# Performance work log

Measured on AMD Instinct MI355X. Metric: run time of the kernel, lower is better.

## Reference

```python
import jax, jax.numpy as jnp
import numpy as np

# Placement region / binning constants (match init_kwargs)
XL, YL, XH, YH = 0.0, 0.0, 512.0, 512.0
NBX, NBY = 512, 512
BSX = (XH - XL) / NBX  # 1.0
BSY = (YH - YL) / NBY  # 1.0
N = 5_000_000  # num_movable_nodes


def setup_inputs() -> dict:
    key = jax.random.key(0)
    k1, k2, k3, k4 = jax.random.split(key, 4)
    # pos = [x_0..x_{N-1}, y_0..y_{N-1}]; keep nodes inside the region
    pos = jax.random.uniform(k1, (2 * N,), jnp.float32) * (XH - 1.0)
    # LUT/FF instances are smaller than one bin -> at most a 2x2 bin window
    node_size_x = jax.random.uniform(k2, (N,), jnp.float32) * 0.9 + 0.05
    node_size_y = jax.random.uniform(k3, (N,), jnp.float32) * 0.9 + 0.05
    utilization_map = jax.random.uniform(k4, (NBX, NBY), jnp.float32) * 2.0
    flop_lut_indices = jnp.arange(N, dtype=jnp.int32)
    return {"pos": pos, "node_size_x": node_size_x, "node_size_y": node_size_y,
            "utilization_map": utilization_map, "flop_lut_indices": flop_lut_indices}


def _route_area(pos, sx, sy, umap):
    x = pos[:N]
    y = pos[N:2 * N]
    x_hi = x + sx
    y_hi = y + sy
    # lowest overlapped bin index per node
    bx0 = jnp.clip(jnp.floor((x - XL) / BSX).astype(jnp.int32), 0, NBX - 1)
    by0 = jnp.clip(jnp.floor((y - YL) / BSY).astype(jnp.int32), 0, NBY - 1)
    area = jnp.zeros((N,), jnp.float32)
    # node extent < bin size => at most a 2x2 window of bins overlaps each node
    for dx in range(2):
        bx = bx0 + dx
        bxl = XL + bx.astype(jnp.float32) * BSX
        ox = jnp.clip(jnp.minimum(x_hi, bxl + BSX) - jnp.maximum(x, bxl), 0.0, None)
        ox = jnp.where(bx < NBX, ox, 0.0)
        bxc = jnp.minimum(bx, NBX - 1)
        for dy in range(2):
            by = by0 + dy
            byl = YL + by.astype(jnp.float32) * BSY
            oy = jnp.clip(jnp.minimum(y_hi, byl + BSY) - jnp.maximum(y, byl), 0.0, None)
            oy = jnp.where(by < NBY, oy, 0.0)
            byc = jnp.minimum(by, NBY - 1)
            # irregular gather from the 2D utilization map
            area = area + ox * oy * umap[bxc, byc]
    return area


def reference(pos, node_size_x, node_size_y, utilization_map, flop_lut_indices):
    area = _route_area(pos, node_size_x, node_size_y, utilization_map)
    # only flop/lut instances receive a route area; others stay zero
    out = jnp.zeros((N,), jnp.float32).at[flop_lut_indices].set(area[flop_lut_indices])
    return out
```

## Files before the change

kernel.cpp:

```cpp
#include <hip/hip_runtime.h>

#define NBX 512
#define NBY 512

__global__ __launch_bounds__(256) void build_table_kernel(
    const float* __restrict__ u, float4* __restrict__ W)
{
    int t = blockIdx.x * blockDim.x + threadIdx.x;
    int bx = t >> 9;
    int by = t & 511;
    int bxp = bx + 1 < NBX ? bx + 1 : NBX - 1;
    int byp = by + 1 < NBY ? by + 1 : NBY - 1;
    float a = u[(bx  << 9) | by ];
    float b = u[(bx  << 9) | byp];
    float c = u[(bxp << 9) | by ];
    float d = u[(bxp << 9) | byp];
    W[t] = make_float4(a, b, c, d);
}

__device__ __forceinline__ float node_area(float x, float y, float sx, float sy,
                                           const float4* __restrict__ W)
{
    float x_hi = x + sx;
    float y_hi = y + sy;

    int bx0 = (int)floorf(x);
    bx0 = bx0 < 0 ? 0 : (bx0 > NBX - 1 ? NBX - 1 : bx0);
    int by0 = (int)floorf(y);
    by0 = by0 < 0 ? 0 : (by0 > NBY - 1 ? NBY - 1 : by0);

    float bx0f = (float)bx0;
    float by0f = (float)by0;

    float ox0 = fmaxf(fminf(x_hi, bx0f + 1.0f) - fmaxf(x, bx0f), 0.0f);
    float ox1 = fmaxf(fminf(x_hi, bx0f + 2.0f) - fmaxf(x, bx0f + 1.0f), 0.0f);
    if (bx0 + 1 >= NBX) ox1 = 0.0f;

    float oy0 = fmaxf(fminf(y_hi, by0f + 1.0f) - fmaxf(y, by0f), 0.0f);
    float oy1 = fmaxf(fminf(y_hi, by0f + 2.0f) - fmaxf(y, by0f + 1.0f), 0.0f);
    if (by0 + 1 >= NBY) oy1 = 0.0f;

    float4 w = W[(bx0 << 9) | by0];

    float area = ox0 * oy0 * w.x;
    area = fmaf(ox0 * oy1, w.y, area);
    area = fmaf(ox1 * oy0, w.z, area);
    area = fmaf(ox1 * oy1, w.w, area);
    return area;
}

__global__ __launch_bounds__(256) void route_area_v2_kernel(
    const float*  __restrict__ pos,
    const float*  __restrict__ nsx,
    const float*  __restrict__ nsy,
    const float4* __restrict__ W,
    const int*    __restrict__ idx,
    float*        __restrict__ out,
    int n)
{
    int t = blockIdx.x * blockDim.x + threadIdx.x;
    int base = t * 4;
    if (base >= n) return;

    if (base + 3 < n) {
        int4 j4 = *(const int4*)(idx + base);
        if (j4.x == base && j4.y == base + 1 && j4.z == base + 2 && j4.w == base + 3) {
            float4 x4  = *(const float4*)(pos + base);
            float4 y4  = *(const float4*)(pos + n + base);
            float4 sx4 = *(const float4*)(nsx + base);
            float4 sy4 = *(const float4*)(nsy + base);

            float4 r;
            r.x = node_area(x4.x, y4.x, sx4.x, sy4.x, W);
            r.y = node_area(x4.y, y4.y, sx4.y, sy4.y, W);
            r.z = node_area(x4.z, y4.z, sx4.z, sy4.z, W);
            r.w = node_area(x4.w, y4.w, sx4.w, sy4.w, W);

            *(float4*)(out + base) = r;
            return;
        }
    }

    #pragma unroll
    for (int k = 0; k < 4; ++k) {
        int i = base + k;
        if (i >= n) break;
        int j = idx[i];
        float x  = pos[j];
        float y  = pos[n + j];
        float sx = nsx[j];
        float sy = nsy[j];
        out[j] = node_area(x, y, sx, sy, W);
    }
}

__global__ __launch_bounds__(256) void route_area_v1_kernel(
    const float* __restrict__ pos,
    const float* __restrict__ nsx,
    const float* __restrict__ nsy,
    const float* __restrict__ umap,
    const int*   __restrict__ idx,
    float*       __restrict__ out,
    int n)
{
    int i = blockIdx.x * blockDim.x + threadIdx.x;
    if (i >= n) return;

    int j = idx[i];
    float x  = pos[j];
    float y  = pos[n + j];
    float sx = nsx[j];
    float sy = nsy[j];
    float x_hi = x + sx;
    float y_hi = y + sy;

    int bx0 = (int)floorf(x);
    bx0 = bx0 < 0 ? 0 : (bx0 > NBX - 1 ? NBX - 1 : bx0);
    int by0 = (int)floorf(y);
    by0 = by0 < 0 ? 0 : (by0 > NBY - 1 ? NBY - 1 : by0);

    float area = 0.0f;
    #pragma unroll
    for (int dx = 0; dx < 2; ++dx) {
        int bx = bx0 + dx;
        float bxl = (float)bx;
        float ox = fmaxf(fminf(x_hi, bxl + 1.0f) - fmaxf(x, bxl), 0.0f);
        if (bx >= NBX) ox = 0.0f;
        int bxc = bx < NBX - 1 ? bx : NBX - 1;
        #pragma unroll
        for (int dy = 0; dy < 2; ++dy) {
            int by = by0 + dy;
            float byl = (float)by;
            float oy = fmaxf(fminf(y_hi, byl + 1.0f) - fmaxf(y, byl), 0.0f);
            if (by >= NBY) oy = 0.0f;
            int byc = by < NBY - 1 ? by : NBY - 1;
            area = fmaf(ox * oy, umap[bxc * NBY + byc], area);
        }
    }
    out[j] = area;
}

extern "C" void kernel_launch(void* const* d_in, const int* in_sizes, int n_in,
                              void* d_out, int out_size, void* d_ws, size_t ws_size,
                              hipStream_t stream)
{
    const float* pos  = (const float*)d_in[0];
    const float* nsx  = (const float*)d_in[1];
    const float* nsy  = (const float*)d_in[2];
    const float* umap = (const float*)d_in[3];
    const int*   idx  = (const int*)d_in[4];
    float* out = (float*)d_out;

    int n = in_sizes[1];

    const size_t table_bytes = (size_t)NBX * NBY * sizeof(float4);

    if (ws_size >= table_bytes) {
        float4* W = (float4*)d_ws;
        build_table_kernel<<<(NBX * NBY) / 256, 256, 0, stream>>>(umap, W);

        int threads = (n + 3) / 4;
        int grid = (threads + 255) / 256;
        route_area_v2_kernel<<<grid, 256, 0, stream>>>(pos, nsx, nsy, W, idx, out, n);
    } else {
        int grid = (n + 255) / 256;
        route_area_v1_kernel<<<grid, 256, 0, stream>>>(pos, nsx, nsy, umap, idx, out, n);
    }
}
```

Before: 160.1 us.

## Store bin table in fp16, process eight nodes per thread with nontemporal loads

The precomputed 2x2 utilization table is stored as half2 pairs (8 bytes per entry instead of 16), which halves the gather footprint so it fits better in cache. Each thread now handles eight nodes. All geometry is computed first, then the eight table gathers are issued together to expose memory-level parallelism. Streaming loads and stores use nontemporal hints to avoid polluting cache. The fp16 table adds rounding error to the utilization values (up to 2.0), which may exceed the tolerance.

```diff
diff --git a/kernel.cpp b/kernel.cpp
--- a/kernel.cpp
+++ b/kernel.cpp
@@ -1,10 +1,16 @@
 #include <hip/hip_runtime.h>
+#include <hip/hip_fp16.h>
 
 #define NBX 512
 #define NBY 512
 
+typedef float vf4 __attribute__((ext_vector_type(4)));
+typedef int   vi4 __attribute__((ext_vector_type(4)));
+
+struct alignas(8) W4 { __half2 ab; __half2 cd; };
+
 __global__ __launch_bounds__(256) void build_table_kernel(
-    const float* __restrict__ u, float4* __restrict__ W)
+    const float* __restrict__ u, W4* __restrict__ W)
 {
     int t = blockIdx.x * blockDim.x + threadIdx.x;
     int bx = t >> 9;
@@ -15,11 +21,15 @@
     float b = u[(bx  << 9) | byp];
     float c = u[(bxp << 9) | by ];
     float d = u[(bxp << 9) | byp];
-    W[t] = make_float4(a, b, c, d);
-}
-
-__device__ __forceinline__ float node_area(float x, float y, float sx, float sy,
-                                           const float4* __restrict__ W)
+    W4 w;
+    w.ab = __floats2half2_rn(a, b);
+    w.cd = __floats2half2_rn(c, d);
+    W[t] = w;
+}
+
+__device__ __forceinline__ void node_geom(float x, float y, float sx, float sy,
+                                          int& addr, float& ox0, float& ox1,
+                                          float& oy0, float& oy1)
 {
     float x_hi = x + sx;
     float y_hi = y + sy;
@@ -32,57 +42,89 @@
     float bx0f = (float)bx0;
     float by0f = (float)by0;
 
-    float ox0 = fmaxf(fminf(x_hi, bx0f + 1.0f) - fmaxf(x, bx0f), 0.0f);
-    float ox1 = fmaxf(fminf(x_hi, bx0f + 2.0f) - fmaxf(x, bx0f + 1.0f), 0.0f);
+    ox0 = fmaxf(fminf(x_hi, bx0f + 1.0f) - fmaxf(x, bx0f), 0.0f);
+    ox1 = fmaxf(fminf(x_hi, bx0f + 2.0f) - fmaxf(x, bx0f + 1.0f), 0.0f);
     if (bx0 + 1 >= NBX) ox1 = 0.0f;
 
-    float oy0 = fmaxf(fminf(y_hi, by0f + 1.0f) - fmaxf(y, by0f), 0.0f);
-    float oy1 = fmaxf(fminf(y_hi, by0f + 2.0f) - fmaxf(y, by0f + 1.0f), 0.0f);
+    oy0 = fmaxf(fminf(y_hi, by0f + 1.0f) - fmaxf(y, by0f), 0.0f);
+    oy1 = fmaxf(fminf(y_hi, by0f + 2.0f) - fmaxf(y, by0f + 1.0f), 0.0f);
     if (by0 + 1 >= NBY) oy1 = 0.0f;
 
-    float4 w = W[(bx0 << 9) | by0];
-
-    float area = ox0 * oy0 * w.x;
-    area = fmaf(ox0 * oy1, w.y, area);
-    area = fmaf(ox1 * oy0, w.z, area);
-    area = fmaf(ox1 * oy1, w.w, area);
+    addr = (bx0 << 9) | by0;
+}
+
+__device__ __forceinline__ float node_eval(W4 w, float ox0, float ox1,
+                                           float oy0, float oy1)
+{
+    float2 f01 = __half22float2(w.ab);
+    float2 f23 = __half22float2(w.cd);
+    float area = ox0 * oy0 * f01.x;
+    area = fmaf(ox0 * oy1, f01.y, area);
+    area = fmaf(ox1 * oy0, f23.x, area);
+    area = fmaf(ox1 * oy1, f23.y, area);
     return area;
 }
 
-__global__ __launch_bounds__(256) void route_area_v2_kernel(
-    const float*  __restrict__ pos,
-    const float*  __restrict__ nsx,
-    const float*  __restrict__ nsy,
-    const float4* __restrict__ W,
-    const int*    __restrict__ idx,
-    float*        __restrict__ out,
+__global__ __launch_bounds__(256) void route_area_v3_kernel(
+    const float* __restrict__ pos,
+    const float* __restrict__ nsx,
+    const float* __restrict__ nsy,
+    const W4*    __restrict__ W,
+    const int*   __restrict__ idx,
+    float*       __restrict__ out,
     int n)
 {
     int t = blockIdx.x * blockDim.x + threadIdx.x;
-    int base = t * 4;
+    int base = t * 8;
     if (base >= n) return;
 
-    if (base + 3 < n) {
-        int4 j4 = *(const int4*)(idx + base);
-        if (j4.x == base && j4.y == base + 1 && j4.z == base + 2 && j4.w == base + 3) {
-            float4 x4  = *(const float4*)(pos + base);
-            float4 y4  = *(const float4*)(pos + n + base);
-            float4 sx4 = *(const float4*)(nsx + base);
-            float4 sy4 = *(const float4*)(nsy + base);
-
-            float4 r;
-            r.x = node_area(x4.x, y4.x, sx4.x, sy4.x, W);
-            r.y = node_area(x4.y, y4.y, sx4.y, sy4.y, W);
-            r.z = node_area(x4.z, y4.z, sx4.z, sy4.z, W);
-            r.w = node_area(x4.w, y4.w, sx4.w, sy4.w, W);
-
-            *(float4*)(out + base) = r;
+    if (base + 7 < n) {
+        vi4 j0 = __builtin_nontemporal_load((const vi4*)(idx + base));
+        vi4 j1 = __builtin_nontemporal_load((const vi4*)(idx + base + 4));
+        bool contig = (j0.x == base)     & (j0.y == base + 1) &
+                      (j0.z == base + 2) & (j0.w == base + 3) &
+                      (j1.x == base + 4) & (j1.y == base + 5) &
+                      (j1.z == base + 6) & (j1.w == base + 7);
+        if (contig) {
+            vf4 xa  = __builtin_nontemporal_load((const vf4*)(pos + base));
+            vf4 xb  = __builtin_nontemporal_load((const vf4*)(pos + base + 4));
+            vf4 ya  = __builtin_nontemporal_load((const vf4*)(pos + n + base));
+            vf4 yb  = __builtin_nontemporal_load((const vf4*)(pos + n + base + 4));
+            vf4 sxa = __builtin_nontemporal_load((const vf4*)(nsx + base));
+            vf4 sxb = __builtin_nontemporal_load((const vf4*)(nsx + base + 4));
+            vf4 sya = __builtin_nontemporal_load((const vf4*)(nsy + base));
+            vf4 syb = __builtin_nontemporal_load((const vf4*)(nsy + base + 4));
+
+            float x[8]  = {xa.x, xa.y, xa.z, xa.w, xb.x, xb.y, xb.z, xb.w};
+            float y[8]  = {ya.x, ya.y, ya.z, ya.w, yb.x, yb.y, yb.z, yb.w};
+            float sx[8] = {sxa.x, sxa.y, sxa.z, sxa.w, sxb.x, sxb.y, sxb.z, sxb.w};
+            float sy[8] = {sya.x, sya.y, sya.z, sya.w, syb.x, syb.y, syb.z, syb.w};
+
+            int   addr[8];
+            float ox0[8], ox1[8], oy0[8], oy1[8];
+            #pragma unroll
+            for (int k = 0; k < 8; ++k)
+                node_geom(x[k], y[k], sx[k], sy[k], addr[k],
+                          ox0[k], ox1[k], oy0[k], oy1[k]);
+
+            W4 w[8];
+            #pragma unroll
+            for (int k = 0; k < 8; ++k) w[k] = W[addr[k]];
+
+            float r[8];
+            #pragma unroll
+            for (int k = 0; k < 8; ++k)
+                r[k] = node_eval(w[k], ox0[k], ox1[k], oy0[k], oy1[k]);
+
+            vf4 ra = {r[0], r[1], r[2], r[3]};
+            vf4 rb = {r[4], r[5], r[6], r[7]};
+            __builtin_nontemporal_store(ra, (vf4*)(out + base));
+            __builtin_nontemporal_store(rb, (vf4*)(out + base + 4));
             return;
         }
     }
 
-    #pragma unroll
-    for (int k = 0; k < 4; ++k) {
+    for (int k = 0; k < 8; ++k) {
         int i = base + k;
         if (i >= n) break;
         int j = idx[i];
@@ -90,7 +132,9 @@
         float y  = pos[n + j];
         float sx = nsx[j];
         float sy = nsy[j];
-        out[j] = node_area(x, y, sx, sy, W);
+        int addr; float ox0, ox1, oy0, oy1;
+        node_geom(x, y, sx, sy, addr, ox0, ox1, oy0, oy1);
+        out[j] = node_eval(W[addr], ox0, ox1, oy0, oy1);
     }
 }
 
@@ -153,15 +197,16 @@
 
     int n = in_sizes[1];
 
-    const size_t table_bytes = (size_t)NBX * NBY * sizeof(float4);
+    const size_t table_bytes = (size_t)NBX * NBY * sizeof(W4);
 
     if (ws_size >= table_bytes) {
-        float4* W = (float4*)d_ws;
+        W4* W = (W4*)d_ws;
         build_table_kernel<<<(NBX * NBY) / 256, 256, 0, stream>>>(umap, W);
 
-        int threads = (n + 3) / 4;
+        int threads = (n + 7) / 8;
         int grid = (threads + 255) / 256;
-        route_area_v2_kernel<<<grid, 256, 0, stream>>>(pos, nsx, nsy, W, idx, out, n);
+        route_area_v3_kernel<<<grid, 256, 0, stream>>>(pos, nsx, nsy, (const W4*)W,
+                                                       idx, out, n);
     } else {
         int grid = (n + 255) / 256;
         route_area_v1_kernel<<<grid, 256, 0, stream>>>(pos, nsx, nsy, umap, idx, out, n);
```

Result: faster. 156.9 us (-2.0%).
